# Optimization experiments

Measured on AMD Instinct MI355X. Metric: run time of the kernel, lower is better.

Reference implementation:

```python
import jax, jax.numpy as jnp
import numpy as np


def setup_inputs() -> dict:
    key = jax.random.key(0)
    ks = jax.random.split(key, 11)
    B, T, I, H, HL = 1024, 512, 2, 256, 256
    s = 0.05
    return {
        "x": jax.random.normal(ks[0], (B, T, I), dtype=jnp.float32),
        "W_ih": jax.random.normal(ks[1], (4 * H, I), dtype=jnp.float32) * s,
        "W_hh": jax.random.normal(ks[2], (4 * H, H), dtype=jnp.float32) * s,
        "b_ih": jax.random.normal(ks[3], (4 * H,), dtype=jnp.float32) * s,
        "b_hh": jax.random.normal(ks[4], (4 * H,), dtype=jnp.float32) * s,
        "W1": jax.random.normal(ks[5], (HL, H), dtype=jnp.float32) * s,
        "b1": jax.random.normal(ks[6], (HL,), dtype=jnp.float32) * s,
        "W2": jax.random.normal(ks[7], (HL, HL), dtype=jnp.float32) * s,
        "b2": jax.random.normal(ks[8], (HL,), dtype=jnp.float32) * s,
        "W3": jax.random.normal(ks[9], (1, HL), dtype=jnp.float32) * s,
        "b3": jax.random.normal(ks[10], (1,), dtype=jnp.float32) * s,
    }


def _lstm_last_hidden(x, W_ih, W_hh, b_ih, b_hh):
    # x: [B, T, I]; PyTorch gate order i, f, g, o packed along 4H.
    B, T, _ = x.shape
    H = W_hh.shape[1]
    # Precompute input contribution to all gates: [T, B, 4H]
    xg = jnp.einsum('bti,gi->tbg', x, W_ih) + b_ih + b_hh

    def step(carry, g_t):
        h, c = carry
        gates = g_t + h @ W_hh.T  # [B, 4H]
        i, f, g, o = jnp.split(gates, 4, axis=-1)
        i = jax.nn.sigmoid(i)
        f = jax.nn.sigmoid(f)
        g = jnp.tanh(g)
        o = jax.nn.sigmoid(o)
        c = f * c + i * g
        h = o * jnp.tanh(c)
        return (h, c), None

    h0 = jnp.zeros((B, H), dtype=x.dtype)
    c0 = jnp.zeros((B, H), dtype=x.dtype)
    (hT, _), _ = jax.lax.scan(step, (h0, c0), xg)
    return hT  # == output[:, -1, :]


def reference(x, W_ih, W_hh, b_ih, b_hh, W1, b1, W2, b2, W3, b3):
    h = _lstm_last_hidden(x, W_ih, W_hh, b_ih, b_hh)  # [B, H]
    out = jax.nn.relu(h @ W1.T + b1)
    out = jax.nn.relu(out @ W2.T + b2)
    out = out @ W3.T + b3  # [B, 1]
    return out
```

## Files before the change

kernel.cpp:

```cpp
#include <hip/hip_runtime.h>
#include <math.h>


typedef __attribute__((ext_vector_type(8))) short bf16x8;
typedef __attribute__((ext_vector_type(4))) float f32x4;

#define MFMA16(a, b, c) __builtin_amdgcn_mfma_f32_16x16x32_bf16((a), (b), (c), 0, 0, 0)

__device__ __forceinline__ ushort f2bf(float f) {
    union { float f; unsigned u; } v; v.f = f;
    unsigned r = v.u + 0x7fffu + ((v.u >> 16) & 1u);
    return (ushort)(r >> 16);
}
__device__ __forceinline__ float bf2f(ushort b) {
    union { unsigned u; float f; } v; v.u = ((unsigned)b) << 16; return v.f;
}
__device__ __forceinline__ float fsig(float x)  { return 1.f / (1.f + __expf(-x)); }
__device__ __forceinline__ float ftanh_(float x){ return 2.f / (1.f + __expf(-2.f * x)) - 1.f; }

__global__ void pack_whh(const float* __restrict__ W, ushort* __restrict__ wf)
{
    const int idx  = blockIdx.x * 256 + threadIdx.x;
    const int lane = idx & 63;
    const int f    = idx >> 6;
    const int gt   = f & 3;
    const int kt   = (f >> 2) & 7;
    const int wv   = f >> 5;
    const int g    = gt * 256 + wv * 16 + (lane & 15);
    const int k0   = kt * 32 + (lane >> 4) * 8;
    const float* src = W + (size_t)g * 256 + k0;
    bf16x8 v;
#pragma unroll
    for (int i = 0; i < 8; ++i) v[i] = (short)f2bf(src[i]);
    *(bf16x8*)(wf + (size_t)idx * 8) = v;
}

__global__ void transpose_kernel(const float* __restrict__ in,
                                 float* __restrict__ out,
                                 int rows, int cols)
{
    __shared__ float tile[32][33];
    const int c0 = blockIdx.x * 32;
    const int r0 = blockIdx.y * 32;
    const int tx = threadIdx.x;
    const int ty = threadIdx.y;
#pragma unroll
    for (int i = 0; i < 4; ++i)
        tile[ty + i * 8][tx] = in[(r0 + ty + i * 8) * cols + (c0 + tx)];
    __syncthreads();
#pragma unroll
    for (int i = 0; i < 4; ++i)
        out[(c0 + ty + i * 8) * rows + (r0 + tx)] = tile[tx][ty + i * 8];
}

__global__ __launch_bounds__(1024)
void lstm_kernel(const float* __restrict__ x,
                 const ushort* __restrict__ wfrag,
                 const float* __restrict__ W_ih,
                 const float* __restrict__ b_ih,
                 const float* __restrict__ b_hh,
                 float* __restrict__ hT)
{
    __shared__ ushort wcache[16 * 8 * 512];
    __shared__ __align__(16) ushort hbuf[2 * 16 * 256];

    const int tid  = threadIdx.x;
    const int lane = tid & 63;
    const int wv   = tid >> 6;
    const int fm   = lane & 15;
    const int fc   = lane >> 4;
    const int br   = blockIdx.x * 16;
    const int u    = wv * 16 + fm;

    float bias[4], wi0[4], wi1[4];
#pragma unroll
    for (int gt = 0; gt < 4; ++gt) {
        const int g = gt * 256 + u;
        bias[gt] = b_ih[g] + b_hh[g];
        wi0[gt]  = W_ih[2 * g + 0];
        wi1[gt]  = W_ih[2 * g + 1];
    }

    for (int i = tid; i < 2 * 16 * 256; i += 1024) hbuf[i] = 0;

    const ushort* wf_wave = wfrag + (size_t)wv * 16384 + lane * 8;
    ushort* wcw = &wcache[(size_t)(wv * 8) * 512 + lane * 8];
#pragma unroll
    for (int q = 0; q < 8; ++q) {
        const bf16x8 v = *(const bf16x8*)(wf_wave + q * 512);
        *(bf16x8*)(wcw + q * 512) = v;
    }

    int aoff[8];
#pragma unroll
    for (int kt = 0; kt < 8; ++kt)
        aoff[kt] = (fm * 512 + kt * 64 + fc * 16) ^ ((fm & 7) << 4);
    int hoff[4];
#pragma unroll
    for (int r = 0; r < 4; ++r) {
        const int row = fc * 4 + r;
        hoff[r] = (row * 512 + u * 2) ^ ((row & 7) << 4);
    }

    const char* hbase = (const char*)hbuf;
    const float* xrow = x + (size_t)br * 1024;

    float c[4] = {0.f, 0.f, 0.f, 0.f};
    __syncthreads();

    for (int t = 0; t < 512; ++t) {
        f32x4 acc[4];
#pragma unroll
        for (int gt = 0; gt < 4; ++gt) acc[gt] = (f32x4){0.f, 0.f, 0.f, 0.f};

        float xr0[4], xr1[4];
#pragma unroll
        for (int r = 0; r < 4; ++r) {
            const float2 xv = *(const float2*)(xrow + (size_t)(fc * 4 + r) * 1024 + 2 * t);
            xr0[r] = xv.x; xr1[r] = xv.y;
        }

        bf16x8 wb0[4], wb1[4];
#pragma unroll
        for (int gt = 0; gt < 4; ++gt) wb0[gt] = *(const bf16x8*)(wf_wave + (8  + gt) * 512);
#pragma unroll
        for (int gt = 0; gt < 4; ++gt) wb1[gt] = *(const bf16x8*)(wf_wave + (12 + gt) * 512);

#pragma unroll
        for (int kt = 0; kt < 2; ++kt) {
            const bf16x8 ah = *(const bf16x8*)(hbase + aoff[kt]);
            const bf16x8 al = *(const bf16x8*)(hbase + aoff[kt] + 8192);
#pragma unroll
            for (int gt = 0; gt < 4; ++gt) {
                const bf16x8 w = *(const bf16x8*)(wcw + (kt * 4 + gt) * 512);
                acc[gt] = MFMA16(ah, w, acc[gt]);
                acc[gt] = MFMA16(al, w, acc[gt]);
            }
        }

#pragma unroll
        for (int kt = 2; kt < 8; ++kt) {
            const bf16x8 ah = *(const bf16x8*)(hbase + aoff[kt]);
            const bf16x8 al = *(const bf16x8*)(hbase + aoff[kt] + 8192);
            if ((kt & 1) == 0) {
#pragma unroll
                for (int gt = 0; gt < 4; ++gt) {
                    acc[gt] = MFMA16(ah, wb0[gt], acc[gt]);
                    acc[gt] = MFMA16(al, wb0[gt], acc[gt]);
                }
                if (kt + 2 < 8) {
#pragma unroll
                    for (int gt = 0; gt < 4; ++gt)
                        wb0[gt] = *(const bf16x8*)(wf_wave + ((kt + 2) * 4 + gt) * 512);
                }
            } else {
#pragma unroll
                for (int gt = 0; gt < 4; ++gt) {
                    acc[gt] = MFMA16(ah, wb1[gt], acc[gt]);
                    acc[gt] = MFMA16(al, wb1[gt], acc[gt]);
                }
                if (kt + 2 < 8) {
#pragma unroll
                    for (int gt = 0; gt < 4; ++gt)
                        wb1[gt] = *(const bf16x8*)(wf_wave + ((kt + 2) * 4 + gt) * 512);
                }
            }
        }
        __syncthreads();

#pragma unroll
        for (int r = 0; r < 4; ++r) {
            const float si = acc[0][r] + fmaf(xr1[r], wi1[0], fmaf(xr0[r], wi0[0], bias[0]));
            const float sf = acc[1][r] + fmaf(xr1[r], wi1[1], fmaf(xr0[r], wi0[1], bias[1]));
            const float sg = acc[2][r] + fmaf(xr1[r], wi1[2], fmaf(xr0[r], wi0[2], bias[2]));
            const float so = acc[3][r] + fmaf(xr1[r], wi1[3], fmaf(xr0[r], wi0[3], bias[3]));
            const float gi = fsig(si);
            const float gf = fsig(sf);
            const float gg = ftanh_(sg);
            const float go = fsig(so);
            c[r] = gf * c[r] + gi * gg;
            const float h = go * ftanh_(c[r]);
            const ushort hh = f2bf(h);
            const ushort hl = f2bf(h - bf2f(hh));
            *(ushort*)((char*)hbuf + hoff[r])        = hh;
            *(ushort*)((char*)hbuf + hoff[r] + 8192) = hl;
            if (t == 511) hT[(size_t)(br + fc * 4 + r) * 256 + u] = h;
        }
        __syncthreads();
    }
}

__global__ void mlp_kernel(const float* __restrict__ hT,
                           const float* __restrict__ W1T,
                           const float* __restrict__ b1,
                           const float* __restrict__ W2T,
                           const float* __restrict__ b2,
                           const float* __restrict__ W3,
                           const float* __restrict__ b3,
                           float* __restrict__ out)
{
    __shared__ float hs[8][256];
    __shared__ float a1[8][256];
    __shared__ float a2[8][256];
    __shared__ float p3[8][257];

    const int tid = threadIdx.x;
    const int br  = blockIdx.x * 8;

#pragma unroll
    for (int r = 0; r < 8; ++r) hs[r][tid] = hT[(size_t)(br + r) * 256 + tid];
    __syncthreads();

    {
        float acc[8];
#pragma unroll
        for (int r = 0; r < 8; ++r) acc[r] = b1[tid];
        for (int k = 0; k < 256; k += 4) {
            const float w0 = W1T[(k + 0) * 256 + tid];
            const float w1 = W1T[(k + 1) * 256 + tid];
            const float w2 = W1T[(k + 2) * 256 + tid];
            const float w3 = W1T[(k + 3) * 256 + tid];
#pragma unroll
            for (int r = 0; r < 8; ++r) {
                const float4 hv = *(const float4*)&hs[r][k];
                acc[r] = fmaf(w0, hv.x, acc[r]);
                acc[r] = fmaf(w1, hv.y, acc[r]);
                acc[r] = fmaf(w2, hv.z, acc[r]);
                acc[r] = fmaf(w3, hv.w, acc[r]);
            }
        }
#pragma unroll
        for (int r = 0; r < 8; ++r) a1[r][tid] = fmaxf(acc[r], 0.f);
    }
    __syncthreads();

    {
        float acc[8];
#pragma unroll
        for (int r = 0; r < 8; ++r) acc[r] = b2[tid];
        for (int k = 0; k < 256; k += 4) {
            const float w0 = W2T[(k + 0) * 256 + tid];
            const float w1 = W2T[(k + 1) * 256 + tid];
            const float w2 = W2T[(k + 2) * 256 + tid];
            const float w3 = W2T[(k + 3) * 256 + tid];
#pragma unroll
            for (int r = 0; r < 8; ++r) {
                const float4 hv = *(const float4*)&a1[r][k];
                acc[r] = fmaf(w0, hv.x, acc[r]);
                acc[r] = fmaf(w1, hv.y, acc[r]);
                acc[r] = fmaf(w2, hv.z, acc[r]);
                acc[r] = fmaf(w3, hv.w, acc[r]);
            }
        }
#pragma unroll
        for (int r = 0; r < 8; ++r) a2[r][tid] = fmaxf(acc[r], 0.f);
    }
    __syncthreads();

    {
        const float w = W3[tid];
#pragma unroll
        for (int r = 0; r < 8; ++r) p3[r][tid] = w * a2[r][tid];
    }
    __syncthreads();
    if (tid < 8) {
        float s = 0.f;
        for (int k = 0; k < 256; ++k) s += p3[tid][k];
        out[br + tid] = s + b3[0];
    }
}

extern "C" void kernel_launch(void* const* d_in, const int* in_sizes, int n_in,
                              void* d_out, int out_size, void* d_ws, size_t ws_size,
                              hipStream_t stream)
{
    const float* x    = (const float*)d_in[0];
    const float* W_ih = (const float*)d_in[1];
    const float* W_hh = (const float*)d_in[2];
    const float* b_ih = (const float*)d_in[3];
    const float* b_hh = (const float*)d_in[4];
    const float* W1   = (const float*)d_in[5];
    const float* b1   = (const float*)d_in[6];
    const float* W2   = (const float*)d_in[7];
    const float* b2   = (const float*)d_in[8];
    const float* W3   = (const float*)d_in[9];
    const float* b3   = (const float*)d_in[10];

    float*  hT    = (float*)d_ws;
    float*  W1T   = hT + 1024 * 256;
    float*  W2T   = W1T + 256 * 256;
    ushort* wfrag = (ushort*)(W2T + 256 * 256);

    pack_whh<<<128, 256, 0, stream>>>(W_hh, wfrag);
    transpose_kernel<<<dim3(8, 8), dim3(32, 8), 0, stream>>>(W1, W1T, 256, 256);
    transpose_kernel<<<dim3(8, 8), dim3(32, 8), 0, stream>>>(W2, W2T, 256, 256);

    lstm_kernel<<<64, 1024, 0, stream>>>(x, wfrag, W_ih, b_ih, b_hh, hT);
    mlp_kernel<<<128, 256, 0, stream>>>(hT, W1T, b1, W2T, b2, W3, b3, (float*)d_out);
}
```

Measured before the change: 3.828 ms.

## Switch LSTM recurrence to single fp16 MFMA with double-buffered hidden state

Result: slower. 4.259 ms (+11.2%).

```diff
diff --git a/kernel.cpp b/kernel.cpp
--- a/kernel.cpp
+++ b/kernel.cpp
@@ -2,23 +2,15 @@
 #include <math.h>
 
 
-typedef __attribute__((ext_vector_type(8))) short bf16x8;
+typedef _Float16 f16x8 __attribute__((ext_vector_type(8)));
 typedef __attribute__((ext_vector_type(4))) float f32x4;
 
-#define MFMA16(a, b, c) __builtin_amdgcn_mfma_f32_16x16x32_bf16((a), (b), (c), 0, 0, 0)
-
-__device__ __forceinline__ ushort f2bf(float f) {
-    union { float f; unsigned u; } v; v.f = f;
-    unsigned r = v.u + 0x7fffu + ((v.u >> 16) & 1u);
-    return (ushort)(r >> 16);
-}
-__device__ __forceinline__ float bf2f(ushort b) {
-    union { unsigned u; float f; } v; v.u = ((unsigned)b) << 16; return v.f;
-}
+#define MFMA16F(a, b, c) __builtin_amdgcn_mfma_f32_16x16x32_f16((a), (b), (c), 0, 0, 0)
+
 __device__ __forceinline__ float fsig(float x)  { return 1.f / (1.f + __expf(-x)); }
 __device__ __forceinline__ float ftanh_(float x){ return 2.f / (1.f + __expf(-2.f * x)) - 1.f; }
 
-__global__ void pack_whh(const float* __restrict__ W, ushort* __restrict__ wf)
+__global__ void pack_whh(const float* __restrict__ W, _Float16* __restrict__ wf)
 {
     const int idx  = blockIdx.x * 256 + threadIdx.x;
     const int lane = idx & 63;
@@ -29,10 +21,10 @@
     const int g    = gt * 256 + wv * 16 + (lane & 15);
     const int k0   = kt * 32 + (lane >> 4) * 8;
     const float* src = W + (size_t)g * 256 + k0;
-    bf16x8 v;
-#pragma unroll
-    for (int i = 0; i < 8; ++i) v[i] = (short)f2bf(src[i]);
-    *(bf16x8*)(wf + (size_t)idx * 8) = v;
+    f16x8 v;
+#pragma unroll
+    for (int i = 0; i < 8; ++i) v[i] = (_Float16)src[i];
+    *(f16x8*)(wf + (size_t)idx * 8) = v;
 }
 
 __global__ void transpose_kernel(const float* __restrict__ in,
@@ -55,14 +47,13 @@
 
 __global__ __launch_bounds__(1024)
 void lstm_kernel(const float* __restrict__ x,
-                 const ushort* __restrict__ wfrag,
+                 const _Float16* __restrict__ wfrag,
                  const float* __restrict__ W_ih,
                  const float* __restrict__ b_ih,
                  const float* __restrict__ b_hh,
                  float* __restrict__ hT)
 {
-    __shared__ ushort wcache[16 * 8 * 512];
-    __shared__ __align__(16) ushort hbuf[2 * 16 * 256];
+    __shared__ __align__(16) _Float16 hbuf[2 * 16 * 256];
 
     const int tid  = threadIdx.x;
     const int lane = tid & 63;
@@ -81,15 +72,13 @@
         wi1[gt]  = W_ih[2 * g + 1];
     }
 
-    for (int i = tid; i < 2 * 16 * 256; i += 1024) hbuf[i] = 0;
-
-    const ushort* wf_wave = wfrag + (size_t)wv * 16384 + lane * 8;
-    ushort* wcw = &wcache[(size_t)(wv * 8) * 512 + lane * 8];
-#pragma unroll
-    for (int q = 0; q < 8; ++q) {
-        const bf16x8 v = *(const bf16x8*)(wf_wave + q * 512);
-        *(bf16x8*)(wcw + q * 512) = v;
-    }
+    for (int i = tid; i < 2 * 16 * 256; i += 1024) hbuf[i] = (_Float16)0.f;
+
+    const _Float16* wf_wave = wfrag + (size_t)wv * 16384 + lane * 8;
+
+    f16x8 wc[8];
+#pragma unroll
+    for (int q = 0; q < 8; ++q) wc[q] = *(const f16x8*)(wf_wave + q * 512);
 
     int aoff[8];
 #pragma unroll
@@ -102,16 +91,21 @@
         hoff[r] = (row * 512 + u * 2) ^ ((row & 7) << 4);
     }
 
-    const char* hbase = (const char*)hbuf;
+    const char* hb = (const char*)hbuf;
     const float* xrow = x + (size_t)br * 1024;
 
+    f16x8 wb0[4], wb1[4];
+#pragma unroll
+    for (int gt = 0; gt < 4; ++gt) wb0[gt] = *(const f16x8*)(wf_wave + (8  + gt) * 512);
+#pragma unroll
+    for (int gt = 0; gt < 4; ++gt) wb1[gt] = *(const f16x8*)(wf_wave + (12 + gt) * 512);
+
     float c[4] = {0.f, 0.f, 0.f, 0.f};
     __syncthreads();
 
     for (int t = 0; t < 512; ++t) {
-        f32x4 acc[4];
-#pragma unroll
-        for (int gt = 0; gt < 4; ++gt) acc[gt] = (f32x4){0.f, 0.f, 0.f, 0.f};
+        const int cur = (t & 1) * 8192;
+        const int nxt = 8192 - cur;
 
         float xr0[4], xr1[4];
 #pragma unroll
@@ -120,53 +114,55 @@
             xr0[r] = xv.x; xr1[r] = xv.y;
         }
 
-        bf16x8 wb0[4], wb1[4];
-#pragma unroll
-        for (int gt = 0; gt < 4; ++gt) wb0[gt] = *(const bf16x8*)(wf_wave + (8  + gt) * 512);
-#pragma unroll
-        for (int gt = 0; gt < 4; ++gt) wb1[gt] = *(const bf16x8*)(wf_wave + (12 + gt) * 512);
+        f32x4 acc[4];
+#pragma unroll
+        for (int gt = 0; gt < 4; ++gt) acc[gt] = (f32x4){0.f, 0.f, 0.f, 0.f};
 
 #pragma unroll
         for (int kt = 0; kt < 2; ++kt) {
-            const bf16x8 ah = *(const bf16x8*)(hbase + aoff[kt]);
-            const bf16x8 al = *(const bf16x8*)(hbase + aoff[kt] + 8192);
-#pragma unroll
-            for (int gt = 0; gt < 4; ++gt) {
-                const bf16x8 w = *(const bf16x8*)(wcw + (kt * 4 + gt) * 512);
-                acc[gt] = MFMA16(ah, w, acc[gt]);
-                acc[gt] = MFMA16(al, w, acc[gt]);
-            }
-        }
-
-#pragma unroll
-        for (int kt = 2; kt < 8; ++kt) {
-            const bf16x8 ah = *(const bf16x8*)(hbase + aoff[kt]);
-            const bf16x8 al = *(const bf16x8*)(hbase + aoff[kt] + 8192);
-            if ((kt & 1) == 0) {
-#pragma unroll
-                for (int gt = 0; gt < 4; ++gt) {
-                    acc[gt] = MFMA16(ah, wb0[gt], acc[gt]);
-                    acc[gt] = MFMA16(al, wb0[gt], acc[gt]);
-                }
-                if (kt + 2 < 8) {
-#pragma unroll
-                    for (int gt = 0; gt < 4; ++gt)
-                        wb0[gt] = *(const bf16x8*)(wf_wave + ((kt + 2) * 4 + gt) * 512);
-                }
-            } else {
-#pragma unroll
-                for (int gt = 0; gt < 4; ++gt) {
-                    acc[gt] = MFMA16(ah, wb1[gt], acc[gt]);
-                    acc[gt] = MFMA16(al, wb1[gt], acc[gt]);
-                }
-                if (kt + 2 < 8) {
-#pragma unroll
-                    for (int gt = 0; gt < 4; ++gt)
-                        wb1[gt] = *(const bf16x8*)(wf_wave + ((kt + 2) * 4 + gt) * 512);
-                }
-            }
-        }
-        __syncthreads();
+            const f16x8 a = *(const f16x8*)(hb + cur + aoff[kt]);
+#pragma unroll
+            for (int gt = 0; gt < 4; ++gt)
+                acc[gt] = MFMA16F(a, wc[kt * 4 + gt], acc[gt]);
+        }
+
+        {
+            const f16x8 a2 = *(const f16x8*)(hb + cur + aoff[2]);
+#pragma unroll
+            for (int gt = 0; gt < 4; ++gt) acc[gt] = MFMA16F(a2, wb0[gt], acc[gt]);
+#pragma unroll
+            for (int gt = 0; gt < 4; ++gt) wb0[gt] = *(const f16x8*)(wf_wave + (16 + gt) * 512);
+
+            const f16x8 a3 = *(const f16x8*)(hb + cur + aoff[3]);
+#pragma unroll
+            for (int gt = 0; gt < 4; ++gt) acc[gt] = MFMA16F(a3, wb1[gt], acc[gt]);
+#pragma unroll
+            for (int gt = 0; gt < 4; ++gt) wb1[gt] = *(const f16x8*)(wf_wave + (20 + gt) * 512);
+
+            const f16x8 a4 = *(const f16x8*)(hb + cur + aoff[4]);
+#pragma unroll
+            for (int gt = 0; gt < 4; ++gt) acc[gt] = MFMA16F(a4, wb0[gt], acc[gt]);
+#pragma unroll
+            for (int gt = 0; gt < 4; ++gt) wb0[gt] = *(const f16x8*)(wf_wave + (24 + gt) * 512);
+
+            const f16x8 a5 = *(const f16x8*)(hb + cur + aoff[5]);
+#pragma unroll
+            for (int gt = 0; gt < 4; ++gt) acc[gt] = MFMA16F(a5, wb1[gt], acc[gt]);
+#pragma unroll
+            for (int gt = 0; gt < 4; ++gt) wb1[gt] = *(const f16x8*)(wf_wave + (28 + gt) * 512);
+
+            const f16x8 a6 = *(const f16x8*)(hb + cur + aoff[6]);
+#pragma unroll
+            for (int gt = 0; gt < 4; ++gt) acc[gt] = MFMA16F(a6, wb0[gt], acc[gt]);
+#pragma unroll
+            for (int gt = 0; gt < 4; ++gt) wb0[gt] = *(const f16x8*)(wf_wave + (8 + gt) * 512);
+
+            const f16x8 a7 = *(const f16x8*)(hb + cur + aoff[7]);
+#pragma unroll
+            for (int gt = 0; gt < 4; ++gt) acc[gt] = MFMA16F(a7, wb1[gt], acc[gt]);
+#pragma unroll
+            for (int gt = 0; gt < 4; ++gt) wb1[gt] = *(const f16x8*)(wf_wave + (12 + gt) * 512);
+        }
 
 #pragma unroll
         for (int r = 0; r < 4; ++r) {
@@ -180,10 +176,7 @@
             const float go = fsig(so);
             c[r] = gf * c[r] + gi * gg;
             const float h = go * ftanh_(c[r]);
-            const ushort hh = f2bf(h);
-            const ushort hl = f2bf(h - bf2f(hh));
-            *(ushort*)((char*)hbuf + hoff[r])        = hh;
-            *(ushort*)((char*)hbuf + hoff[r] + 8192) = hl;
+            *(_Float16*)((char*)hbuf + nxt + hoff[r]) = (_Float16)h;
             if (t == 511) hT[(size_t)(br + fc * 4 + r) * 256 + u] = h;
         }
         __syncthreads();
@@ -286,10 +279,10 @@
     const float* W3   = (const float*)d_in[9];
     const float* b3   = (const float*)d_in[10];
 
-    float*  hT    = (float*)d_ws;
-    float*  W1T   = hT + 1024 * 256;
-    float*  W2T   = W1T + 256 * 256;
-    ushort* wfrag = (ushort*)(W2T + 256 * 256);
+    float*     hT    = (float*)d_ws;
+    float*     W1T   = hT + 1024 * 256;
+    float*     W2T   = W1T + 256 * 256;
+    _Float16*  wfrag = (_Float16*)(W2T + 256 * 256);
 
     pack_whh<<<128, 256, 0, stream>>>(W_hh, wfrag);
     transpose_kernel<<<dim3(8, 8), dim3(32, 8), 0, stream>>>(W1, W1T, 256, 256);
```
